# Performance work log

Measured on AMD Instinct MI355X. Metric: run time of the kernel, lower is better.

The kernel has to match this reference:

```python
import jax, jax.numpy as jnp
import numpy as np

KS = 3          # kernel_size
NK = KS * KS    # sample points per output pixel
PAD = KS // 2   # 'same' zero padding


def setup_inputs() -> dict:
    key = jax.random.key(0)
    k1, k2, k3, k4 = jax.random.split(key, 4)
    B, H, W, C, F = 8, 64, 64, 128, 256
    x = jax.random.normal(k1, (B, H, W, C), jnp.float32)
    offset = jax.random.normal(k2, (B, H, W, 2 * NK), jnp.float32)
    modulation = jax.random.uniform(k3, (B, H, W, NK), jnp.float32)
    conv_kernel = jax.random.normal(k4, (KS, KS, C, F), jnp.float32) * 0.02
    conv_bias = jnp.zeros((F,), jnp.float32)
    return {"x": x, "offset": offset, "modulation": modulation,
            "conv_kernel": conv_kernel, "conv_bias": conv_bias}


def reference(x, offset, modulation, conv_kernel, conv_bias):
    B, H, W, C = x.shape
    # zero pad ('same')
    xp = jnp.pad(x, ((0, 0), (PAD, PAD), (PAD, PAD), (0, 0)))
    ih, iw = H + 2 * PAD, W + 2 * PAD

    # offset: first NK channels are y-offsets, last NK are x-offsets -> [B,H,W,NK,2]
    off = jnp.stack([offset[..., :NK], offset[..., NK:]], axis=-1)

    # pixel centers in padded coords (start at 1 due to padding), stride 1
    gy, gx = jnp.meshgrid(jnp.arange(1, H + 1), jnp.arange(1, W + 1), indexing="ij")
    pix = jnp.stack([gy, gx], -1).reshape(1, H, W, 1, 2).astype(x.dtype)

    # kernel tap offsets, ky varies slowest after flatten (matches TF source)
    ky, kx = jnp.meshgrid(jnp.arange(-PAD, KS - PAD), jnp.arange(-PAD, KS - PAD), indexing="ij")
    ker = jnp.stack([ky.reshape(-1), kx.reshape(-1)], -1).reshape(1, 1, 1, NK, 2).astype(x.dtype)

    p = off + pix + ker                       # [B,H,W,NK,2] sampling locations
    y0f = jnp.floor(p[..., 0])
    x0f = jnp.floor(p[..., 1])
    y0 = jnp.clip(y0f, 0, ih - 1)
    x0 = jnp.clip(x0f, 0, iw - 1)
    y1 = jnp.clip(y0f + 1.0, 0, ih - 1)
    x1 = jnp.clip(x0f + 1.0, 0, iw - 1)

    bidx = jnp.arange(B).reshape(B, 1, 1, 1)

    def gather(yi, xi):  # -> [B,H,W,NK,C]
        return xp[bidx, yi.astype(jnp.int32), xi.astype(jnp.int32)]

    f00 = gather(y0, x0)
    f01 = gather(y1, x0)
    f10 = gather(y0, x1)
    f11 = gather(y1, x1)

    py = jnp.clip(p[..., 0], 0, ih - 1)[..., None]
    px = jnp.clip(p[..., 1], 0, iw - 1)[..., None]
    ly = py - y0[..., None]
    lx = px - x0[..., None]

    feats = ((1.0 - ly) * (1.0 - lx) * f00 + (1.0 - ly) * lx * f01
             + ly * (1.0 - lx) * f10 + ly * lx * f11)      # [B,H,W,NK,C]
    feats = feats * modulation[..., None]

    # rearrange exactly as the TF code: concat kernel-row chunks along H, then reshape
    feats = jnp.concatenate([feats[:, :, :, s:s + KS, :] for s in range(0, NK, KS)], axis=1)
    feats = feats.reshape(B, H * KS, W * KS, C)

    out = jax.lax.conv_general_dilated(
        feats, conv_kernel, window_strides=(KS, KS), padding="VALID",
        dimension_numbers=("NHWC", "HWIO", "NHWC"))
    return out + conv_bias
```

## Files before the change

kernel.cpp:

```cpp
#include <hip/hip_runtime.h>

typedef __attribute__((ext_vector_type(8))) short short8;
typedef __attribute__((ext_vector_type(4))) float f32x4;

__device__ __forceinline__ unsigned short f2bf(float f) {
  union { float f; unsigned u; } v; v.f = f;
  unsigned r = v.u + 0x7FFFu + ((v.u >> 16) & 1u);
  return (unsigned short)(r >> 16);
}

__device__ __forceinline__ short8 pack8(f32x4 a, f32x4 b) {
  short8 p;
  p[0] = (short)f2bf(a.x); p[1] = (short)f2bf(a.y);
  p[2] = (short)f2bf(a.z); p[3] = (short)f2bf(a.w);
  p[4] = (short)f2bf(b.x); p[5] = (short)f2bf(b.y);
  p[6] = (short)f2bf(b.z); p[7] = (short)f2bf(b.w);
  return p;
}

constexpr int KKt = 1152;
constexpr int Ff  = 256;

__global__ void wt_prep(const float* __restrict__ kf, unsigned short* __restrict__ wtB) {
  int idx = blockIdx.x * 256 + threadIdx.x;
  int j  = idx & 7;
  int fr = (idx >> 3) & 15;
  int kg = (idx >> 7) & 3;
  int ft = (idx >> 9) & 15;
  int ks = (idx >> 13) & 3;
  int ch = idx >> 15;
  int k = ch * 128 + ks * 32 + kg * 8 + j;
  int f = ft * 16 + fr;
  wtB[idx] = f2bf(kf[k * Ff + f]);
}

__global__ __launch_bounds__(512, 4) void dcn_main(
    const float* __restrict__ x, const float* __restrict__ off,
    const float* __restrict__ mo, const unsigned short* __restrict__ wtB,
    const float* __restrict__ bias, float* __restrict__ out) {
  __shared__ __align__(16) char At[2][64 * 272];

  const int b  = blockIdx.x & 7;
  const int oh = blockIdx.x >> 3;
  const int t  = threadIdx.x;
  const int lane = t & 63;
  const int wv   = t >> 6;
  const int fr   = lane & 15;
  const int kg   = lane >> 4;
  const int sow  = t >> 3;
  const int c16  = t & 7;

  f32x4 acc[4][2];
#pragma unroll
  for (int i = 0; i < 4; ++i) { acc[i][0] = f32x4{0,0,0,0}; acc[i][1] = f32x4{0,0,0,0}; }

  float oyr[2], oxr[2], mmr[2];
  int   og[4]; float wg[4];

  auto loadOff = [&](int ch, int sl) {
    const int dy = ch / 3, dxk = ch - dy * 3;
    const int r = 3 * oh + dy, hp = r & 63, kp = ((r >> 6) * 3) + dxk;
    const int pix = (b * 64 + hp) * 64 + sow;
    oyr[sl] = off[pix * 18 + kp];
    oxr[sl] = off[pix * 18 + 9 + kp];
    mmr[sl] = mo[pix * 9 + kp];
  };

  auto calcW = [&](int ch, int sl) {
    const int dy = ch / 3, dxk = ch - dy * 3;
    const int r = 3 * oh + dy, hp = r & 63, kp = ((r >> 6) * 3) + dxk;
    const float py = oyr[sl] + (float)(hp + kp / 3);
    const float px = oxr[sl] + (float)(sow + kp % 3);
    const float mm = mmr[sl];
    const float y0f = floorf(py), x0f = floorf(px);
    const float y0 = fminf(fmaxf(y0f, 0.f), 65.f);
    const float y1 = fminf(fmaxf(y0f + 1.f, 0.f), 65.f);
    const float x0 = fminf(fmaxf(x0f, 0.f), 65.f);
    const float x1 = fminf(fmaxf(x0f + 1.f, 0.f), 65.f);
    const float ly = fminf(fmaxf(py, 0.f), 65.f) - y0;
    const float lx = fminf(fmaxf(px, 0.f), 65.f) - x0;
    wg[0] = (1.f - ly) * (1.f - lx) * mm;
    wg[1] = (1.f - ly) * lx * mm;
    wg[2] = ly * (1.f - lx) * mm;
    wg[3] = ly * lx * mm;
    const int iy0 = (int)y0, iy1 = (int)y1, ix0 = (int)x0, ix1 = (int)x1;
    const int yy[4] = {iy0, iy1, iy0, iy1};
    const int xx[4] = {ix0, ix0, ix1, ix1};
#pragma unroll
    for (int j = 0; j < 4; ++j) {
      const bool v = (yy[j] >= 1) & (yy[j] <= 64) & (xx[j] >= 1) & (xx[j] <= 64);
      int o = ((b * 64 + yy[j] - 1) * 64 + (xx[j] - 1)) * 128 + c16 * 16;
      if (!v) { o = 0; wg[j] = 0.f; }
      og[j] = o;
    }
  };

  auto ldC = [&](int c, f32x4* G) {
    const f32x4* p = (const f32x4*)(x + og[c]);
    G[0] = p[0]; G[1] = p[1]; G[2] = p[2]; G[3] = p[3];
  };

  auto ldB = [&](int ch, int ks, short8* bf) {
    const unsigned short* p = wtB + (((ch * 4 + ks) * 16 + wv * 2) * 64 + lane) * 8;
    bf[0] = *(const short8*)p;
    bf[1] = *(const short8*)(p + 512);
  };

  auto mmah = [&](int buf, int ks, const short8* bf) {
    short8 af[4];
#pragma unroll
    for (int m2 = 0; m2 < 4; ++m2)
      af[m2] = *(const short8*)(At[buf] + (m2 * 16 + fr) * 272 + ks * 64 + kg * 16);
#pragma unroll
    for (int m2 = 0; m2 < 4; ++m2)
#pragma unroll
      for (int nb = 0; nb < 2; ++nb)
        acc[m2][nb] = __builtin_amdgcn_mfma_f32_16x16x32_bf16(af[m2], bf[nb], acc[m2][nb], 0, 0, 0);
  };

  const int wb = sow * 272 + c16 * 32;

  loadOff(0, 0); loadOff(1, 1);
  calcW(0, 0);
  {
    f32x4 G0[4], G1[4];
    ldC(0, G0); ldC(1, G1);
    f32x4 P0 = wg[0]*G0[0] + wg[1]*G1[0], P1 = wg[0]*G0[1] + wg[1]*G1[1];
    f32x4 P2 = wg[0]*G0[2] + wg[1]*G1[2], P3 = wg[0]*G0[3] + wg[1]*G1[3];
    ldC(2, G0); ldC(3, G1);
    P0 += wg[2]*G0[0] + wg[3]*G1[0]; P1 += wg[2]*G0[1] + wg[3]*G1[1];
    P2 += wg[2]*G0[2] + wg[3]*G1[2]; P3 += wg[2]*G0[3] + wg[3]*G1[3];
    *(short8*)(At[0] + wb)      = pack8(P0, P1);
    *(short8*)(At[0] + wb + 16) = pack8(P2, P3);
  }
  __syncthreads();

#pragma unroll
  for (int ch = 0; ch < 9; ++ch) {
    const int buf = ch & 1;
    const bool hv = ch < 8;
    if (hv) calcW(ch + 1, (ch + 1) & 1);
    short8 bA[2], bB[2];
    f32x4 G0[4], G1[4], P0, P1, P2, P3;
    ldB(ch, 0, bA);
    if (hv) ldC(0, G0);
    ldB(ch, 1, bB);
    mmah(buf, 0, bA);
    if (hv) { P0 = wg[0]*G0[0]; P1 = wg[0]*G0[1]; P2 = wg[0]*G0[2]; P3 = wg[0]*G0[3]; }
    if (hv) ldC(1, G1);
    ldB(ch, 2, bA);
    mmah(buf, 1, bB);
    if (hv) { P0 += wg[1]*G1[0]; P1 += wg[1]*G1[1]; P2 += wg[1]*G1[2]; P3 += wg[1]*G1[3]; }
    if (hv) ldC(2, G0);
    ldB(ch, 3, bB);
    if (ch < 7) loadOff(ch + 2, ch & 1);
    mmah(buf, 2, bA);
    if (hv) { P0 += wg[2]*G0[0]; P1 += wg[2]*G0[1]; P2 += wg[2]*G0[2]; P3 += wg[2]*G0[3]; }
    if (hv) ldC(3, G1);
    mmah(buf, 3, bB);
    if (hv) {
      P0 += wg[3]*G1[0]; P1 += wg[3]*G1[1]; P2 += wg[3]*G1[2]; P3 += wg[3]*G1[3];
      *(short8*)(At[buf ^ 1] + wb)      = pack8(P0, P1);
      *(short8*)(At[buf ^ 1] + wb + 16) = pack8(P2, P3);
      __syncthreads();
    }
  }

  float bs[2];
#pragma unroll
  for (int nb = 0; nb < 2; ++nb) bs[nb] = bias[wv * 32 + nb * 16 + fr];
  float* orow = out + (long)(b * 64 + oh) * 64 * 256;
#pragma unroll
  for (int m2 = 0; m2 < 4; ++m2) {
#pragma unroll
    for (int j = 0; j < 4; ++j) {
      const int ow = m2 * 16 + kg * 4 + j;
#pragma unroll
      for (int nb = 0; nb < 2; ++nb)
        orow[ow * 256 + wv * 32 + nb * 16 + fr] = acc[m2][nb][j] + bs[nb];
    }
  }
}

extern "C" void kernel_launch(void* const* d_in, const int* in_sizes, int n_in,
                              void* d_out, int out_size, void* d_ws, size_t ws_size,
                              hipStream_t stream) {
  const float* x    = (const float*)d_in[0];
  const float* off  = (const float*)d_in[1];
  const float* mo   = (const float*)d_in[2];
  const float* kf   = (const float*)d_in[3];
  const float* bias = (const float*)d_in[4];
  float* outp = (float*)d_out;
  unsigned short* wtB = (unsigned short*)d_ws;

  wt_prep<<<1152, 256, 0, stream>>>(kf, wtB);
  dcn_main<<<512, 512, 0, stream>>>(x, off, mo, wtB, bias, outp);
}
```

Measured before the change: 58.68 us.

## Pre-convert input features to bf16 so the gather moves half the bytes

Adds a prep kernel that converts x to bf16 in workspace, and a templated main-kernel path that gathers bf16 corner values, unpacks them to fp32 for the bilinear blend, and packs the result back. It also moves the A-tile store before the last MFMA stage and makes the barrier unconditional. The goal is to halve gather traffic in the memory-bound bilinear sampling. The cost is an extra full pass over x (read 32MB, write 16MB) and bf16 rounding of the inputs before interpolation. The old fp32 path remains as a fallback when the workspace is too small.

```diff
diff --git a/kernel.cpp b/kernel.cpp
--- a/kernel.cpp
+++ b/kernel.cpp
@@ -20,6 +20,8 @@
 
 constexpr int KKt = 1152;
 constexpr int Ff  = 256;
+constexpr size_t WT_BYTES = (size_t)KKt * Ff * 2;
+constexpr size_t XB_BYTES = (size_t)8 * 64 * 64 * 128 * 2;
 
 __global__ void wt_prep(const float* __restrict__ kf, unsigned short* __restrict__ wtB) {
   int idx = blockIdx.x * 256 + threadIdx.x;
@@ -34,8 +36,15 @@
   wtB[idx] = f2bf(kf[k * Ff + f]);
 }
 
+__global__ void x_prep(const float* __restrict__ x, unsigned short* __restrict__ xb) {
+  int i = (blockIdx.x * 512 + threadIdx.x) * 8;
+  const f32x4* p = (const f32x4*)(x + i);
+  *(short8*)(xb + i) = pack8(p[0], p[1]);
+}
+
+template <bool BX>
 __global__ __launch_bounds__(512, 4) void dcn_main(
-    const float* __restrict__ x, const float* __restrict__ off,
+    const void* __restrict__ xsrc, const float* __restrict__ off,
     const float* __restrict__ mo, const unsigned short* __restrict__ wtB,
     const float* __restrict__ bias, float* __restrict__ out) {
   __shared__ __align__(16) char At[2][64 * 272];
@@ -95,11 +104,6 @@
     }
   };
 
-  auto ldC = [&](int c, f32x4* G) {
-    const f32x4* p = (const f32x4*)(x + og[c]);
-    G[0] = p[0]; G[1] = p[1]; G[2] = p[2]; G[3] = p[3];
-  };
-
   auto ldB = [&](int ch, int ks, short8* bf) {
     const unsigned short* p = wtB + (((ch * 4 + ks) * 16 + wv * 2) * 64 + lane) * 8;
     bf[0] = *(const short8*)p;
@@ -120,48 +124,128 @@
 
   const int wb = sow * 272 + c16 * 32;
 
-  loadOff(0, 0); loadOff(1, 1);
-  calcW(0, 0);
-  {
-    f32x4 G0[4], G1[4];
-    ldC(0, G0); ldC(1, G1);
-    f32x4 P0 = wg[0]*G0[0] + wg[1]*G1[0], P1 = wg[0]*G0[1] + wg[1]*G1[1];
-    f32x4 P2 = wg[0]*G0[2] + wg[1]*G1[2], P3 = wg[0]*G0[3] + wg[1]*G1[3];
-    ldC(2, G0); ldC(3, G1);
-    P0 += wg[2]*G0[0] + wg[3]*G1[0]; P1 += wg[2]*G0[1] + wg[3]*G1[1];
-    P2 += wg[2]*G0[2] + wg[3]*G1[2]; P3 += wg[2]*G0[3] + wg[3]*G1[3];
-    *(short8*)(At[0] + wb)      = pack8(P0, P1);
-    *(short8*)(At[0] + wb + 16) = pack8(P2, P3);
-  }
-  __syncthreads();
-
-#pragma unroll
-  for (int ch = 0; ch < 9; ++ch) {
-    const int buf = ch & 1;
-    const bool hv = ch < 8;
-    if (hv) calcW(ch + 1, (ch + 1) & 1);
-    short8 bA[2], bB[2];
-    f32x4 G0[4], G1[4], P0, P1, P2, P3;
-    ldB(ch, 0, bA);
-    if (hv) ldC(0, G0);
-    ldB(ch, 1, bB);
-    mmah(buf, 0, bA);
-    if (hv) { P0 = wg[0]*G0[0]; P1 = wg[0]*G0[1]; P2 = wg[0]*G0[2]; P3 = wg[0]*G0[3]; }
-    if (hv) ldC(1, G1);
-    ldB(ch, 2, bA);
-    mmah(buf, 1, bB);
-    if (hv) { P0 += wg[1]*G1[0]; P1 += wg[1]*G1[1]; P2 += wg[1]*G1[2]; P3 += wg[1]*G1[3]; }
-    if (hv) ldC(2, G0);
-    ldB(ch, 3, bB);
-    if (ch < 7) loadOff(ch + 2, ch & 1);
-    mmah(buf, 2, bA);
-    if (hv) { P0 += wg[2]*G0[0]; P1 += wg[2]*G0[1]; P2 += wg[2]*G0[2]; P3 += wg[2]*G0[3]; }
-    if (hv) ldC(3, G1);
-    mmah(buf, 3, bB);
-    if (hv) {
-      P0 += wg[3]*G1[0]; P1 += wg[3]*G1[1]; P2 += wg[3]*G1[2]; P3 += wg[3]*G1[3];
-      *(short8*)(At[buf ^ 1] + wb)      = pack8(P0, P1);
-      *(short8*)(At[buf ^ 1] + wb + 16) = pack8(P2, P3);
+  if constexpr (BX) {
+    const unsigned short* xb = (const unsigned short*)xsrc;
+    auto ldQ = [&](int c, short8* q) {
+      const short8* p = (const short8*)(xb + og[c]);
+      q[0] = p[0]; q[1] = p[1];
+    };
+    auto accQ = [&](short8 s, float w, f32x4& Pe, f32x4& Po) {
+      union { short8 s; unsigned u[4]; } v; v.s = s;
+#pragma unroll
+      for (int i = 0; i < 4; ++i) {
+        union { unsigned u; float f; } e, o;
+        e.u = v.u[i] << 16;
+        o.u = v.u[i] & 0xffff0000u;
+        Pe[i] = fmaf(w, e.f, Pe[i]);
+        Po[i] = fmaf(w, o.f, Po[i]);
+      }
+    };
+
+    loadOff(0, 0); loadOff(1, 1);
+    calcW(0, 0);
+    {
+      short8 q0[2], q1[2], q2[2], q3[2];
+      ldQ(0, q0); ldQ(1, q1); ldQ(2, q2); ldQ(3, q3);
+      f32x4 Pe0{0,0,0,0}, Po0{0,0,0,0}, Pe1{0,0,0,0}, Po1{0,0,0,0};
+      accQ(q0[0], wg[0], Pe0, Po0); accQ(q0[1], wg[0], Pe1, Po1);
+      accQ(q1[0], wg[1], Pe0, Po0); accQ(q1[1], wg[1], Pe1, Po1);
+      accQ(q2[0], wg[2], Pe0, Po0); accQ(q2[1], wg[2], Pe1, Po1);
+      accQ(q3[0], wg[3], Pe0, Po0); accQ(q3[1], wg[3], Pe1, Po1);
+      short8 s0, s1;
+      s0[0]=f2bf(Pe0.x); s0[1]=f2bf(Po0.x); s0[2]=f2bf(Pe0.y); s0[3]=f2bf(Po0.y);
+      s0[4]=f2bf(Pe0.z); s0[5]=f2bf(Po0.z); s0[6]=f2bf(Pe0.w); s0[7]=f2bf(Po0.w);
+      s1[0]=f2bf(Pe1.x); s1[1]=f2bf(Po1.x); s1[2]=f2bf(Pe1.y); s1[3]=f2bf(Po1.y);
+      s1[4]=f2bf(Pe1.z); s1[5]=f2bf(Po1.z); s1[6]=f2bf(Pe1.w); s1[7]=f2bf(Po1.w);
+      *(short8*)(At[0] + wb)      = s0;
+      *(short8*)(At[0] + wb + 16) = s1;
+    }
+    __syncthreads();
+
+#pragma unroll
+    for (int ch = 0; ch < 9; ++ch) {
+      const int buf = ch & 1;
+      const bool hv = ch < 8;
+      short8 bA[2], bB[2];
+      short8 q0[2], q1[2], q2[2], q3[2];
+      f32x4 Pe0{0,0,0,0}, Po0{0,0,0,0}, Pe1{0,0,0,0}, Po1{0,0,0,0};
+      if (hv) calcW(ch + 1, (ch + 1) & 1);
+      ldB(ch, 0, bA);
+      if (hv) { ldQ(0, q0); ldQ(1, q1); }
+      ldB(ch, 1, bB);
+      mmah(buf, 0, bA);
+      if (hv) {
+        ldQ(2, q2); ldQ(3, q3);
+        accQ(q0[0], wg[0], Pe0, Po0); accQ(q0[1], wg[0], Pe1, Po1);
+      }
+      ldB(ch, 2, bA);
+      mmah(buf, 1, bB);
+      if (hv) { accQ(q1[0], wg[1], Pe0, Po0); accQ(q1[1], wg[1], Pe1, Po1); }
+      ldB(ch, 3, bB);
+      if (ch < 7) loadOff(ch + 2, ch & 1);
+      mmah(buf, 2, bA);
+      if (hv) {
+        accQ(q2[0], wg[2], Pe0, Po0); accQ(q2[1], wg[2], Pe1, Po1);
+        accQ(q3[0], wg[3], Pe0, Po0); accQ(q3[1], wg[3], Pe1, Po1);
+        short8 s0, s1;
+        s0[0]=f2bf(Pe0.x); s0[1]=f2bf(Po0.x); s0[2]=f2bf(Pe0.y); s0[3]=f2bf(Po0.y);
+        s0[4]=f2bf(Pe0.z); s0[5]=f2bf(Po0.z); s0[6]=f2bf(Pe0.w); s0[7]=f2bf(Po0.w);
+        s1[0]=f2bf(Pe1.x); s1[1]=f2bf(Po1.x); s1[2]=f2bf(Pe1.y); s1[3]=f2bf(Po1.y);
+        s1[4]=f2bf(Pe1.z); s1[5]=f2bf(Po1.z); s1[6]=f2bf(Pe1.w); s1[7]=f2bf(Po1.w);
+        *(short8*)(At[buf ^ 1] + wb)      = s0;
+        *(short8*)(At[buf ^ 1] + wb + 16) = s1;
+      }
+      mmah(buf, 3, bB);
+      __syncthreads();
+    }
+  } else {
+    const float* x = (const float*)xsrc;
+    auto ldC = [&](int c, f32x4* G) {
+      const f32x4* p = (const f32x4*)(x + og[c]);
+      G[0] = p[0]; G[1] = p[1]; G[2] = p[2]; G[3] = p[3];
+    };
+    loadOff(0, 0); loadOff(1, 1);
+    calcW(0, 0);
+    {
+      f32x4 G0[4], G1[4];
+      ldC(0, G0); ldC(1, G1);
+      f32x4 P0 = wg[0]*G0[0] + wg[1]*G1[0], P1 = wg[0]*G0[1] + wg[1]*G1[1];
+      f32x4 P2 = wg[0]*G0[2] + wg[1]*G1[2], P3 = wg[0]*G0[3] + wg[1]*G1[3];
+      ldC(2, G0); ldC(3, G1);
+      P0 += wg[2]*G0[0] + wg[3]*G1[0]; P1 += wg[2]*G0[1] + wg[3]*G1[1];
+      P2 += wg[2]*G0[2] + wg[3]*G1[2]; P3 += wg[2]*G0[3] + wg[3]*G1[3];
+      *(short8*)(At[0] + wb)      = pack8(P0, P1);
+      *(short8*)(At[0] + wb + 16) = pack8(P2, P3);
+    }
+    __syncthreads();
+#pragma unroll
+    for (int ch = 0; ch < 9; ++ch) {
+      const int buf = ch & 1;
+      const bool hv = ch < 8;
+      if (hv) calcW(ch + 1, (ch + 1) & 1);
+      short8 bA[2], bB[2];
+      f32x4 G0[4], G1[4], P0, P1, P2, P3;
+      ldB(ch, 0, bA);
+      if (hv) ldC(0, G0);
+      ldB(ch, 1, bB);
+      mmah(buf, 0, bA);
+      if (hv) { P0 = wg[0]*G0[0]; P1 = wg[0]*G0[1]; P2 = wg[0]*G0[2]; P3 = wg[0]*G0[3]; }
+      if (hv) ldC(1, G1);
+      ldB(ch, 2, bA);
+      mmah(buf, 1, bB);
+      if (hv) { P0 += wg[1]*G1[0]; P1 += wg[1]*G1[1]; P2 += wg[1]*G1[2]; P3 += wg[1]*G1[3]; }
+      if (hv) ldC(2, G0);
+      ldB(ch, 3, bB);
+      if (ch < 7) loadOff(ch + 2, ch & 1);
+      mmah(buf, 2, bA);
+      if (hv) { P0 += wg[2]*G0[0]; P1 += wg[2]*G0[1]; P2 += wg[2]*G0[2]; P3 += wg[2]*G0[3]; }
+      if (hv) ldC(3, G1);
+      mmah(buf, 3, bB);
+      if (hv) {
+        P0 += wg[3]*G1[0]; P1 += wg[3]*G1[1]; P2 += wg[3]*G1[2]; P3 += wg[3]*G1[3];
+        *(short8*)(At[buf ^ 1] + wb)      = pack8(P0, P1);
+        *(short8*)(At[buf ^ 1] + wb + 16) = pack8(P2, P3);
+      }
       __syncthreads();
     }
   }
@@ -194,5 +278,11 @@
   unsigned short* wtB = (unsigned short*)d_ws;
 
   wt_prep<<<1152, 256, 0, stream>>>(kf, wtB);
-  dcn_main<<<512, 512, 0, stream>>>(x, off, mo, wtB, bias, outp);
-}
+  if (ws_size >= WT_BYTES + XB_BYTES) {
+    unsigned short* xb = (unsigned short*)((char*)d_ws + WT_BYTES);
+    x_prep<<<1024, 512, 0, stream>>>(x, xb);
+    dcn_main<true><<<512, 512, 0, stream>>>(xb, off, mo, wtB, bias, outp);
+  } else {
+    dcn_main<false><<<512, 512, 0, stream>>>(x, off, mo, wtB, bias, outp);
+  }
+}
```

Result: faster. 51.47 us (-12.3%).

## Pre-convert input to bf16 and gather half-width samples with 1024-thread blocks

Applied to the files above, without the earlier changes.

Adds a pre-pass that converts x to bf16 in the workspace, so the bilinear gather in the main kernel reads half the bytes per sample. The main kernel now runs 16 waves per block, each owning a 32x32 output slice, and each thread handles 8 channels and unpacks bf16 pairs with bit shifts. The old fp32 path stays as a fallback used when the workspace is too small. The cost is an extra full pass over x on every call, an extra rounding of the inputs before interpolation, and higher per-block thread count.

```diff
diff --git a/kernel.cpp b/kernel.cpp
--- a/kernel.cpp
+++ b/kernel.cpp
@@ -18,8 +18,19 @@
   return p;
 }
 
+__device__ __forceinline__ short8 packEO(f32x4 e, f32x4 o) {
+  short8 p;
+  p[0] = (short)f2bf(e.x); p[1] = (short)f2bf(o.x);
+  p[2] = (short)f2bf(e.y); p[3] = (short)f2bf(o.y);
+  p[4] = (short)f2bf(e.z); p[5] = (short)f2bf(o.z);
+  p[6] = (short)f2bf(e.w); p[7] = (short)f2bf(o.w);
+  return p;
+}
+
 constexpr int KKt = 1152;
 constexpr int Ff  = 256;
+constexpr size_t WT_BYTES = (size_t)KKt * Ff * 2;
+constexpr size_t XB_BYTES = (size_t)8 * 64 * 64 * 128 * 2;
 
 __global__ void wt_prep(const float* __restrict__ kf, unsigned short* __restrict__ wtB) {
   int idx = blockIdx.x * 256 + threadIdx.x;
@@ -34,8 +45,14 @@
   wtB[idx] = f2bf(kf[k * Ff + f]);
 }
 
-__global__ __launch_bounds__(512, 4) void dcn_main(
-    const float* __restrict__ x, const float* __restrict__ off,
+__global__ void x_prep(const float* __restrict__ x, unsigned short* __restrict__ xb) {
+  int i = (blockIdx.x * 512 + threadIdx.x) * 8;
+  const f32x4* p = (const f32x4*)(x + i);
+  *(short8*)(xb + i) = pack8(p[0], p[1]);
+}
+
+__global__ __launch_bounds__(1024, 8) void dcn_bf16(
+    const unsigned short* __restrict__ xb, const float* __restrict__ off,
     const float* __restrict__ mo, const unsigned short* __restrict__ wtB,
     const float* __restrict__ bias, float* __restrict__ out) {
   __shared__ __align__(16) char At[2][64 * 272];
@@ -45,14 +62,16 @@
   const int t  = threadIdx.x;
   const int lane = t & 63;
   const int wv   = t >> 6;
+  const int mh   = wv & 1;
+  const int fq   = wv >> 1;
   const int fr   = lane & 15;
   const int kg   = lane >> 4;
-  const int sow  = t >> 3;
-  const int c16  = t & 7;
-
-  f32x4 acc[4][2];
-#pragma unroll
-  for (int i = 0; i < 4; ++i) { acc[i][0] = f32x4{0,0,0,0}; acc[i][1] = f32x4{0,0,0,0}; }
+  const int sow  = t >> 4;
+  const int c8   = t & 15;
+
+  f32x4 acc[2][2];
+#pragma unroll
+  for (int i = 0; i < 2; ++i) { acc[i][0] = f32x4{0,0,0,0}; acc[i][1] = f32x4{0,0,0,0}; }
 
   float oyr[2], oxr[2], mmr[2];
   int   og[4]; float wg[4];
@@ -89,23 +108,161 @@
 #pragma unroll
     for (int j = 0; j < 4; ++j) {
       const bool v = (yy[j] >= 1) & (yy[j] <= 64) & (xx[j] >= 1) & (xx[j] <= 64);
+      int o = ((b * 64 + yy[j] - 1) * 64 + (xx[j] - 1)) * 128 + c8 * 8;
+      if (!v) { o = 0; wg[j] = 0.f; }
+      og[j] = o;
+    }
+  };
+
+  auto ldQ = [&](int c) -> short8 {
+    return *(const short8*)(xb + og[c]);
+  };
+  auto accQ = [&](short8 s, float w, f32x4& Pe, f32x4& Po) {
+    union { short8 s; unsigned u[4]; } v; v.s = s;
+#pragma unroll
+    for (int i = 0; i < 4; ++i) {
+      union { unsigned u; float f; } e, o;
+      e.u = v.u[i] << 16;
+      o.u = v.u[i] & 0xffff0000u;
+      Pe[i] = fmaf(w, e.f, Pe[i]);
+      Po[i] = fmaf(w, o.f, Po[i]);
+    }
+  };
+
+  auto mmah = [&](int buf, int ch, int ks) {
+    const unsigned short* bp = wtB + (((ch * 4 + ks) * 16 + fq * 2) * 64 + lane) * 8;
+    short8 bf0 = *(const short8*)bp;
+    short8 bf1 = *(const short8*)(bp + 512);
+    short8 af[2];
+#pragma unroll
+    for (int m2 = 0; m2 < 2; ++m2)
+      af[m2] = *(const short8*)(At[buf] + (mh * 32 + m2 * 16 + fr) * 272 + ks * 64 + kg * 16);
+#pragma unroll
+    for (int m2 = 0; m2 < 2; ++m2) {
+      acc[m2][0] = __builtin_amdgcn_mfma_f32_16x16x32_bf16(af[m2], bf0, acc[m2][0], 0, 0, 0);
+      acc[m2][1] = __builtin_amdgcn_mfma_f32_16x16x32_bf16(af[m2], bf1, acc[m2][1], 0, 0, 0);
+    }
+  };
+
+  const int wb = sow * 272 + c8 * 16;
+
+  loadOff(0, 0); loadOff(1, 1);
+  calcW(0, 0);
+  {
+    short8 q0 = ldQ(0), q1 = ldQ(1), q2 = ldQ(2), q3 = ldQ(3);
+    f32x4 Pe{0,0,0,0}, Po{0,0,0,0};
+    accQ(q0, wg[0], Pe, Po); accQ(q1, wg[1], Pe, Po);
+    accQ(q2, wg[2], Pe, Po); accQ(q3, wg[3], Pe, Po);
+    *(short8*)(At[0] + wb) = packEO(Pe, Po);
+  }
+  __syncthreads();
+
+#pragma unroll
+  for (int ch = 0; ch < 9; ++ch) {
+    const int buf = ch & 1;
+    const bool hv = ch < 8;
+    short8 q0, q1, q2, q3;
+    f32x4 Pe{0,0,0,0}, Po{0,0,0,0};
+    if (hv) {
+      calcW(ch + 1, (ch + 1) & 1);
+      q0 = ldQ(0); q1 = ldQ(1);
+    }
+    mmah(buf, ch, 0);
+    if (hv) {
+      q2 = ldQ(2); q3 = ldQ(3);
+      accQ(q0, wg[0], Pe, Po);
+    }
+    mmah(buf, ch, 1);
+    if (hv) accQ(q1, wg[1], Pe, Po);
+    if (ch < 7) loadOff(ch + 2, ch & 1);
+    mmah(buf, ch, 2);
+    if (hv) {
+      accQ(q2, wg[2], Pe, Po);
+      accQ(q3, wg[3], Pe, Po);
+      *(short8*)(At[buf ^ 1] + wb) = packEO(Pe, Po);
+    }
+    mmah(buf, ch, 3);
+    __syncthreads();
+  }
+
+  float bs[2];
+#pragma unroll
+  for (int nb = 0; nb < 2; ++nb) bs[nb] = bias[fq * 32 + nb * 16 + fr];
+  float* orow = out + (long)(b * 64 + oh) * 64 * 256;
+#pragma unroll
+  for (int m2 = 0; m2 < 2; ++m2) {
+#pragma unroll
+    for (int j = 0; j < 4; ++j) {
+      const int row = mh * 32 + m2 * 16 + kg * 4 + j;
+#pragma unroll
+      for (int nb = 0; nb < 2; ++nb)
+        orow[row * 256 + fq * 32 + nb * 16 + fr] = acc[m2][nb][j] + bs[nb];
+    }
+  }
+}
+
+__global__ __launch_bounds__(512, 4) void dcn_f32(
+    const float* __restrict__ x, const float* __restrict__ off,
+    const float* __restrict__ mo, const unsigned short* __restrict__ wtB,
+    const float* __restrict__ bias, float* __restrict__ out) {
+  __shared__ __align__(16) char At[2][64 * 272];
+  const int b  = blockIdx.x & 7;
+  const int oh = blockIdx.x >> 3;
+  const int t  = threadIdx.x;
+  const int lane = t & 63;
+  const int wv   = t >> 6;
+  const int fr   = lane & 15;
+  const int kg   = lane >> 4;
+  const int sow  = t >> 3;
+  const int c16  = t & 7;
+
+  f32x4 acc[4][2];
+#pragma unroll
+  for (int i = 0; i < 4; ++i) { acc[i][0] = f32x4{0,0,0,0}; acc[i][1] = f32x4{0,0,0,0}; }
+  float oyr[2], oxr[2], mmr[2];
+  int   og[4]; float wg[4];
+
+  auto loadOff = [&](int ch, int sl) {
+    const int dy = ch / 3, dxk = ch - dy * 3;
+    const int r = 3 * oh + dy, hp = r & 63, kp = ((r >> 6) * 3) + dxk;
+    const int pix = (b * 64 + hp) * 64 + sow;
+    oyr[sl] = off[pix * 18 + kp];
+    oxr[sl] = off[pix * 18 + 9 + kp];
+    mmr[sl] = mo[pix * 9 + kp];
+  };
+  auto calcW = [&](int ch, int sl) {
+    const int dy = ch / 3, dxk = ch - dy * 3;
+    const int r = 3 * oh + dy, hp = r & 63, kp = ((r >> 6) * 3) + dxk;
+    const float py = oyr[sl] + (float)(hp + kp / 3);
+    const float px = oxr[sl] + (float)(sow + kp % 3);
+    const float mm = mmr[sl];
+    const float y0f = floorf(py), x0f = floorf(px);
+    const float y0 = fminf(fmaxf(y0f, 0.f), 65.f);
+    const float y1 = fminf(fmaxf(y0f + 1.f, 0.f), 65.f);
+    const float x0 = fminf(fmaxf(x0f, 0.f), 65.f);
+    const float x1 = fminf(fmaxf(x0f + 1.f, 0.f), 65.f);
+    const float ly = fminf(fmaxf(py, 0.f), 65.f) - y0;
+    const float lx = fminf(fmaxf(px, 0.f), 65.f) - x0;
+    wg[0] = (1.f - ly) * (1.f - lx) * mm;
+    wg[1] = (1.f - ly) * lx * mm;
+    wg[2] = ly * (1.f - lx) * mm;
+    wg[3] = ly * lx * mm;
+    const int iy0 = (int)y0, iy1 = (int)y1, ix0 = (int)x0, ix1 = (int)x1;
+    const int yy[4] = {iy0, iy1, iy0, iy1};
+    const int xx[4] = {ix0, ix0, ix1, ix1};
+#pragma unroll
+    for (int j = 0; j < 4; ++j) {
+      const bool v = (yy[j] >= 1) & (yy[j] <= 64) & (xx[j] >= 1) & (xx[j] <= 64);
       int o = ((b * 64 + yy[j] - 1) * 64 + (xx[j] - 1)) * 128 + c16 * 16;
       if (!v) { o = 0; wg[j] = 0.f; }
       og[j] = o;
     }
   };
-
-  auto ldC = [&](int c, f32x4* G) {
-    const f32x4* p = (const f32x4*)(x + og[c]);
-    G[0] = p[0]; G[1] = p[1]; G[2] = p[2]; G[3] = p[3];
-  };
-
   auto ldB = [&](int ch, int ks, short8* bf) {
     const unsigned short* p = wtB + (((ch * 4 + ks) * 16 + wv * 2) * 64 + lane) * 8;
     bf[0] = *(const short8*)p;
     bf[1] = *(const short8*)(p + 512);
   };
-
   auto mmah = [&](int buf, int ks, const short8* bf) {
     short8 af[4];
 #pragma unroll
@@ -117,9 +274,11 @@
       for (int nb = 0; nb < 2; ++nb)
         acc[m2][nb] = __builtin_amdgcn_mfma_f32_16x16x32_bf16(af[m2], bf[nb], acc[m2][nb], 0, 0, 0);
   };
-
+  auto ldC = [&](int c, f32x4* G) {
+    const f32x4* p = (const f32x4*)(x + og[c]);
+    G[0] = p[0]; G[1] = p[1]; G[2] = p[2]; G[3] = p[3];
+  };
   const int wb = sow * 272 + c16 * 32;
-
   loadOff(0, 0); loadOff(1, 1);
   calcW(0, 0);
   {
@@ -134,7 +293,6 @@
     *(short8*)(At[0] + wb + 16) = pack8(P2, P3);
   }
   __syncthreads();
-
 #pragma unroll
   for (int ch = 0; ch < 9; ++ch) {
     const int buf = ch & 1;
@@ -162,10 +320,9 @@
       P0 += wg[3]*G1[0]; P1 += wg[3]*G1[1]; P2 += wg[3]*G1[2]; P3 += wg[3]*G1[3];
       *(short8*)(At[buf ^ 1] + wb)      = pack8(P0, P1);
       *(short8*)(At[buf ^ 1] + wb + 16) = pack8(P2, P3);
-      __syncthreads();
-    }
-  }
-
+    }
+    __syncthreads();
+  }
   float bs[2];
 #pragma unroll
   for (int nb = 0; nb < 2; ++nb) bs[nb] = bias[wv * 32 + nb * 16 + fr];
@@ -194,5 +351,11 @@
   unsigned short* wtB = (unsigned short*)d_ws;
 
   wt_prep<<<1152, 256, 0, stream>>>(kf, wtB);
-  dcn_main<<<512, 512, 0, stream>>>(x, off, mo, wtB, bias, outp);
-}
+  if (ws_size >= WT_BYTES + XB_BYTES) {
+    unsigned short* xb = (unsigned short*)((char*)d_ws + WT_BYTES);
+    x_prep<<<1024, 512, 0, stream>>>(x, xb);
+    dcn_bf16<<<512, 1024, 0, stream>>>(xb, off, mo, wtB, bias, outp);
+  } else {
+    dcn_f32<<<512, 512, 0, stream>>>(x, off, mo, wtB, bias, outp);
+  }
+}
```

Measured after the change: 57.05 us. 1.03x faster.
